# Kernel tuning notes

Measured on AMD Instinct MI355X. Metric: run time of the kernel, lower is better.

## Reference

```python
import jax, jax.numpy as jnp
import numpy as np

BLKQ = 64
BLKK = 64
TOPK_RATIO = 0.125


def setup_inputs() -> dict:
    key = jax.random.key(0)
    ks = jax.random.split(key, 4)
    B, L, H, D = 1, 4096, 16, 64
    q = jax.random.normal(ks[0], (B, L, H, D), jnp.float32)
    k = jax.random.normal(ks[1], (B, L, H, D), jnp.float32)
    v = jax.random.normal(ks[2], (B, L, H, D), jnp.float32)
    w_proj = jax.random.normal(ks[3], (D, D), jnp.float32) * 0.02
    b_proj = jnp.zeros((D,), jnp.float32)
    return {"q": q, "k": k, "v": v, "w_proj": w_proj, "b_proj": b_proj}


def _sparse_linear_attn(q, k, v, w_proj, b_proj):
    # q,k,v: (B, L, H, D) -> (B, H, L, D)
    q = jnp.transpose(q, (0, 2, 1, 3))
    k = jnp.transpose(k, (0, 2, 1, 3))
    v = jnp.transpose(v, (0, 2, 1, 3))
    B, H, L, D = q.shape
    M, N = L // BLKQ, L // BLKK  # L chosen divisible by block sizes (no padding)
    T = max(1, int(TOPK_RATIO * N))  # selected key blocks per query block

    qb = q.reshape(B, H, M, BLKQ, D)
    kb = k.reshape(B, H, N, BLKK, D)
    vb = v.reshape(B, H, N, BLKK, D)

    # --- block map: mean-pooled block descriptors, topk key blocks per query block ---
    qm = qb.mean(axis=3)  # (B,H,M,D)
    km = kb.mean(axis=3)  # (B,H,N,D)
    blk_scores = jnp.einsum('bhmd,bhnd->bhmn', qm, km)
    _, lut = jax.lax.top_k(blk_scores, T)  # (B,H,M,T) int32

    # --- gather selected K/V blocks ---
    b_idx = jnp.arange(B)[:, None, None, None]
    h_idx = jnp.arange(H)[None, :, None, None]
    k_sel = kb[b_idx, h_idx, lut]  # (B,H,M,T,BLKK,D)
    v_sel = vb[b_idx, h_idx, lut]  # (B,H,M,T,BLKK,D)

    # --- block-sparse softmax attention over gathered keys only ---
    scale = D ** (-0.5)
    att = jnp.einsum('bhmqd,bhmtkd->bhmqtk', qb, k_sel) * scale
    att = att.reshape(B, H, M, BLKQ, T * BLKK)
    p = jax.nn.softmax(att, axis=-1)
    o_s = jnp.einsum('bhmqn,bhmnd->bhmqd', p, v_sel.reshape(B, H, M, T * BLKK, D))
    o_s = o_s.reshape(B, H, L, D)

    # --- global linear attention with softmax feature map ---
    q_fm = jax.nn.softmax(q, axis=-1)
    k_fm = jax.nn.softmax(k, axis=-1)
    kvsum = jnp.einsum('bhld,bhle->bhde', k_fm, v)  # (B,H,D,D)
    ksum = k_fm.sum(axis=2)  # (B,H,D)
    num = jnp.einsum('bhld,bhde->bhle', q_fm, kvsum)
    den = jnp.einsum('bhld,bhd->bhl', q_fm, ksum)[..., None] + 1e-6
    o_l = num / den
    o_l = jnp.einsum('bhld,ed->bhle', o_l, w_proj) + b_proj  # nn.Linear: x @ W.T + b

    o = o_s + o_l
    return jnp.transpose(o, (0, 2, 1, 3))  # (B, L, H, D)


def reference(q, k, v, w_proj, b_proj):
    return _sparse_linear_attn(q, k, v, w_proj, b_proj)
```

## Files before the change

kernel.cpp:

```cpp
#include <hip/hip_runtime.h>


#define NH   16
#define DH   64
#define NBLK 64
#define TSEL 8

typedef unsigned short u16;
typedef unsigned int   u32;
typedef __attribute__((ext_vector_type(8))) short short8;
typedef __attribute__((ext_vector_type(4))) float f4;
typedef __attribute__((ext_vector_type(4))) u32 u32x4;

#define MFMA_BF16(a, b, c) __builtin_amdgcn_mfma_f32_16x16x32_bf16(a, b, c, 0, 0, 0)

__device__ __forceinline__ u16 f2bf_rne(float f) {
  u32 u = __float_as_uint(f);
  u += 0x7fffu + ((u >> 16) & 1u);
  return (u16)(u >> 16);
}
__device__ __forceinline__ u32 pk2(float a, float b) {
  return (u32)f2bf_rne(a) | ((u32)f2bf_rne(b) << 16);
}
__device__ __forceinline__ float bf2f(u16 u) { return __uint_as_float(((u32)u) << 16); }

__device__ __forceinline__ short8 frag_row(const u16* t, int row, int jblk) {
  return *(const short8*)((const char*)t + row * 128 + ((jblk ^ (row & 7)) * 16));
}

__global__ __launch_bounds__(256) void prep_kernel(const float* __restrict__ k,
                                                   const float* __restrict__ v,
                                                   u16* __restrict__ kT,
                                                   u16* __restrict__ vT,
                                                   float* __restrict__ kvp,
                                                   float* __restrict__ ksp,
                                                   float* __restrict__ kmv) {
  __shared__ __align__(16) char vsl[8192];
  __shared__ __align__(16) char kfm[8192];
  __shared__ float kcol[64 * 65];
  __shared__ float redmx[256];
  __shared__ float redsm[256];
  __shared__ float kmred[256];
  __shared__ float ksred[256];
  int b = blockIdx.x;
  int n = (b >> 3) & 63;
  int h = 2 * (b & 7) + (b >> 9);
  int tid = threadIdx.x;
  int w = tid >> 6, lane = tid & 63;
  int row = lane, qd = w;
  int lq = lane & 15, quad = lane >> 4;

  float kv[16];
  {
    const float* kr = k + (size_t)(n * 64 + row) * 1024 + h * 64 + qd * 16;
#pragma unroll
    for (int c4 = 0; c4 < 4; c4++) {
      float4 a = *(const float4*)(kr + c4 * 4);
      kv[c4 * 4] = a.x; kv[c4 * 4 + 1] = a.y; kv[c4 * 4 + 2] = a.z; kv[c4 * 4 + 3] = a.w;
    }
  }
  {
    char* ktb = (char*)(kT + ((size_t)(h * 64 + n)) * 4096);
    uint4 w0 = make_uint4(pk2(kv[0], kv[1]), pk2(kv[2], kv[3]),
                          pk2(kv[4], kv[5]), pk2(kv[6], kv[7]));
    uint4 w1 = make_uint4(pk2(kv[8], kv[9]), pk2(kv[10], kv[11]),
                          pk2(kv[12], kv[13]), pk2(kv[14], kv[15]));
    *(uint4*)(ktb + row * 128 + (((2 * qd) ^ (row & 7)) * 16)) = w0;
    *(uint4*)(ktb + row * 128 + (((2 * qd + 1) ^ (row & 7)) * 16)) = w1;
  }
  {
#pragma unroll
    for (int j = 0; j < 16; j++) kcol[(qd * 16 + j) * 65 + row] = kv[j];
  }
  {
    const float* vr = v + (size_t)(n * 64 + row) * 1024 + h * 64 + qd * 16;
    int kb = row >> 3, klo = row & 7;
#pragma unroll
    for (int c4 = 0; c4 < 4; c4++) {
      float4 a = *(const float4*)(vr + c4 * 4);
      float vv[4] = {a.x, a.y, a.z, a.w};
#pragma unroll
      for (int jj = 0; jj < 4; jj++) {
        int e = qd * 16 + c4 * 4 + jj;
        *(u16*)(vsl + e * 128 + ((kb ^ (e & 7)) * 16) + klo * 2) = f2bf_rne(vv[jj]);
      }
    }
  }
  {
    float mx = kv[0];
#pragma unroll
    for (int j = 1; j < 16; j++) mx = fmaxf(mx, kv[j]);
    redmx[qd * 64 + row] = mx;
  }
  __syncthreads();
  {
    int c = tid & 63, g = tid >> 6;
    float pk = 0.f;
#pragma unroll
    for (int i = 0; i < 16; i++) pk += kcol[c * 65 + g * 16 + i];
    kmred[g * 64 + c] = pk;
  }
  {
    float mx = fmaxf(fmaxf(redmx[row], redmx[64 + row]),
                     fmaxf(redmx[128 + row], redmx[192 + row]));
    float sm = 0.f;
#pragma unroll
    for (int j = 0; j < 16; j++) { kv[j] = __expf(kv[j] - mx); sm += kv[j]; }
    redsm[qd * 64 + row] = sm;
  }
  __syncthreads();
  if (tid < 64)
    kmv[h * 4096 + n * 64 + tid] =
        (kmred[tid] + kmred[64 + tid] + kmred[128 + tid] + kmred[192 + tid]) * (1.0f / 64.0f);
  {
    float sm = redsm[row] + redsm[64 + row] + redsm[128 + row] + redsm[192 + row];
    float inv = 1.0f / sm;
    int rb = row >> 3, rlo = row & 7;
#pragma unroll
    for (int j = 0; j < 16; j++) {
      int d = qd * 16 + j;
      *(u16*)(kfm + d * 128 + (((rb) ^ (d & 7)) * 16) + rlo * 2) = f2bf_rne(kv[j] * inv);
    }
  }
  __syncthreads();

  {
    uint4* vt_out = (uint4*)(vT + ((size_t)(h * 64 + n)) * 4096);
    vt_out[tid] = ((const uint4*)vsl)[tid];
    vt_out[256 + tid] = ((const uint4*)vsl)[256 + tid];
  }
  {
    float ks = 0.f;
    short8 x0 = frag_row((const u16*)kfm, lane, 2 * w);
    short8 x1 = frag_row((const u16*)kfm, lane, 2 * w + 1);
#pragma unroll
    for (int e = 0; e < 8; e++) ks += bf2f((u16)x0[e]) + bf2f((u16)x1[e]);
    ksred[tid] = ks;
  }
  {
    f4 acc[4];
    f4 zz = {0.f, 0.f, 0.f, 0.f};
#pragma unroll
    for (int et = 0; et < 4; et++) acc[et] = zz;
#pragma unroll
    for (int ks2 = 0; ks2 < 2; ks2++) {
      short8 a_ = frag_row((const u16*)kfm, w * 16 + lq, 4 * ks2 + quad);
#pragma unroll
      for (int et = 0; et < 4; et++)
        acc[et] = MFMA_BF16(a_, frag_row((const u16*)vsl, et * 16 + lq, 4 * ks2 + quad), acc[et]);
    }
    float* kvb = kvp + ((size_t)(h * 64 + n)) * 4096;
#pragma unroll
    for (int r = 0; r < 4; r++)
#pragma unroll
      for (int et = 0; et < 4; et++)
        kvb[(w * 16 + quad * 4 + r) * 64 + et * 16 + lq] = acc[et][r];
  }
  __syncthreads();
  if (tid < 64)
    ksp[((size_t)(h * 64 + n)) * 64 + tid] = ksred[tid] + ksred[64 + tid] +
                                             ksred[128 + tid] + ksred[192 + tid];
}

__global__ __launch_bounds__(256) void post_kernel(const float* __restrict__ kvp,
                                                   const float* __restrict__ ksp,
                                                   const float* __restrict__ wgt,
                                                   u16* __restrict__ m2t,
                                                   float* __restrict__ ksum) {
  __shared__ float kr[4][64];
  __shared__ float wl[64 * 65];
  int bx = blockIdx.x, tid = threadIdx.x;
  int h = bx >> 4, dq = bx & 15;
  int j = tid & 63, rr = tid >> 6;

  {
    size_t off = (size_t)(dq * 4 + rr) * 64 + j;
    const float* base = kvp + (size_t)h * 64 * 4096 + off;
    float s0 = 0.f, s1 = 0.f, s2 = 0.f, s3 = 0.f;
#pragma unroll
    for (int n4 = 0; n4 < 16; n4++) {
      s0 += base[(size_t)(n4 * 4 + 0) * 4096];
      s1 += base[(size_t)(n4 * 4 + 1) * 4096];
      s2 += base[(size_t)(n4 * 4 + 2) * 4096];
      s3 += base[(size_t)(n4 * 4 + 3) * 4096];
    }
    kr[rr][j] = (s0 + s1) + (s2 + s3);
  }
#pragma unroll
  for (int i = 0; i < 16; i++) {
    int f = i * 256 + tid;
    wl[(f >> 6) * 65 + (f & 63)] = wgt[f];
  }
  __syncthreads();

  {
    int e = tid & 63, rr2 = tid >> 6;
    float acc = 0.f;
#pragma unroll
    for (int jj = 0; jj < 64; jj++) acc = fmaf(kr[rr2][jj], wl[e * 65 + jj], acc);
    int d = dq * 4 + rr2;
    *(u16*)((char*)m2t + (size_t)h * 8192 + e * 128 +
            (((d >> 3) ^ (e & 7)) * 16) + (d & 7) * 2) = f2bf_rne(acc);
  }
  if (dq == 0 && tid < 64) {
    const float* base = ksp + (size_t)h * 64 * 64 + tid;
    float s = 0.f;
#pragma unroll
    for (int n = 0; n < 64; n++) s += base[(size_t)n * 64];
    ksum[h * 64 + tid] = s;
  }
}

__global__ __launch_bounds__(256, 6) void fused_attn_kernel(const float* __restrict__ q,
                                                            const u16* __restrict__ kT,
                                                            const u16* __restrict__ vT,
                                                            const float* __restrict__ kmv,
                                                            const u16* __restrict__ m2t,
                                                            const float* __restrict__ ksum,
                                                            const float* __restrict__ bproj,
                                                            float* __restrict__ out) {
  __shared__ __align__(16) char smem[24576];
  int b = blockIdx.x;
  int m = (b >> 3) & 63;
  int h = 2 * (b & 7) + (b >> 9);
  int tid = threadIdx.x, w = tid >> 6, lane = tid & 63;
  int lq = lane & 15, quad = lane >> 4;
  char* buf = smem;
  char* p_b = smem + 16384 + w * 2048;
  float* km_s = (float*)smem;
  float* qmp = (float*)(smem + 20480);
  float* qmf = (float*)(smem + 21504);

  {
    int c = tid & 63, g = tid >> 6;
    const float* qcol = q + ((size_t)(m * 64 + g * 16)) * 1024 + h * 64 + c;
    float qp = 0.f;
#pragma unroll
    for (int i = 0; i < 16; i++) qp += qcol[(size_t)i * 1024];
    qmp[g * 64 + c] = qp;
#pragma unroll
    for (int i = 0; i < 16; i++) {
      int idx = i * 256 + tid;
      km_s[(idx >> 6) * 65 + (idx & 63)] = kmv[h * 4096 + idx];
    }
  }
  __syncthreads();
  if (tid < 64) qmf[tid] = qmp[tid] + qmp[64 + tid] + qmp[128 + tid] + qmp[192 + tid];
  __syncthreads();
  int blks[8];
  {
    int n = lane;
    float s = 0.f;
#pragma unroll
    for (int d = 0; d < 64; d++) s += qmf[d] * km_s[n * 65 + d];
    float my = s;
#pragma unroll
    for (int t = 0; t < TSEL; t++) {
      float vv = my; int idx = n;
#pragma unroll
      for (int off = 1; off < 64; off <<= 1) {
        float ov = __shfl_xor(vv, off);
        int oi = __shfl_xor(idx, off);
        if (ov > vv || (ov == vv && oi < idx)) { vv = ov; idx = oi; }
      }
      int sel = __builtin_amdgcn_readfirstlane(idx);
      blks[t] = sel;
      if (n == sel) my = -INFINITY;
    }
  }
  __syncthreads();

  const int qrow = w * 16 + lq;
  const float* qr_g = q + ((size_t)(m * 64 + qrow)) * 1024 + h * 64;
  short8 qf[2];
#pragma unroll
  for (int ks = 0; ks < 2; ks++) {
    const float* gp = qr_g + (4 * ks + quad) * 8;
    float4 a = *(const float4*)gp;
    float4 bb = *(const float4*)(gp + 4);
    u32x4 tt = {pk2(a.x, a.y), pk2(a.z, a.w), pk2(bb.x, bb.y), pk2(bb.z, bb.w)};
    qf[ks] = __builtin_bit_cast(short8, tt);
  }

  {
    const uint4* kt0 = (const uint4*)(kT + ((size_t)(h * 64 + blks[0])) * 4096);
    const uint4* vt0 = (const uint4*)(vT + ((size_t)(h * 64 + blks[0])) * 4096);
    ((uint4*)buf)[tid] = kt0[tid];
    ((uint4*)buf)[256 + tid] = kt0[256 + tid];
    ((uint4*)(buf + 8192))[tid] = vt0[tid];
    ((uint4*)(buf + 8192))[256 + tid] = vt0[256 + tid];
  }
  __syncthreads();

  float mrun = -INFINITY, lrun = 0.f;
  f4 o[4];
  f4 zz = {0.f, 0.f, 0.f, 0.f};
#pragma unroll
  for (int et = 0; et < 4; et++) o[et] = zz;

  const u16* kc = (const u16*)buf;
  const u16* vc = (const u16*)(buf + 8192);

  for (int t = 0; t < 8; t++) {
    uint4 pk0, pk1, pv0, pv1;
    if (t < 7) {
      const uint4* ktn = (const uint4*)(kT + ((size_t)(h * 64 + blks[t + 1])) * 4096);
      const uint4* vtn = (const uint4*)(vT + ((size_t)(h * 64 + blks[t + 1])) * 4096);
      pk0 = ktn[tid]; pk1 = ktn[256 + tid];
      pv0 = vtn[tid]; pv1 = vtn[256 + tid];
    }

    f4 s[4];
#pragma unroll
    for (int kt = 0; kt < 4; kt++) s[kt] = zz;
    __builtin_amdgcn_s_setprio(1);
#pragma unroll
    for (int ks = 0; ks < 2; ks++)
#pragma unroll
      for (int kt = 0; kt < 4; kt++)
        s[kt] = MFMA_BF16(frag_row(kc, kt * 16 + lq, 4 * ks + quad), qf[ks], s[kt]);
    __builtin_amdgcn_s_setprio(0);

    float mp = -INFINITY;
#pragma unroll
    for (int kt = 0; kt < 4; kt++)
#pragma unroll
      for (int r = 0; r < 4; r++) mp = fmaxf(mp, s[kt][r]);
    mp = fmaxf(mp, __shfl_xor(mp, 16));
    mp = fmaxf(mp, __shfl_xor(mp, 32));
    mp *= 0.125f;
    if (__any(mp > mrun)) {
      float mn = fmaxf(mrun, mp);
      float al = __expf(mrun - mn);
      mrun = mn;
      lrun *= al;
#pragma unroll
      for (int et = 0; et < 4; et++)
#pragma unroll
        for (int r = 0; r < 4; r++) o[et][r] *= al;
    }
    float rs_ = 0.f;
#pragma unroll
    for (int kt = 0; kt < 4; kt++) {
      float p0 = __expf(fmaf(s[kt][0], 0.125f, -mrun));
      float p1 = __expf(fmaf(s[kt][1], 0.125f, -mrun));
      float p2 = __expf(fmaf(s[kt][2], 0.125f, -mrun));
      float p3 = __expf(fmaf(s[kt][3], 0.125f, -mrun));
      rs_ += p0 + p1 + p2 + p3;
      u32 lo32 = (__float_as_uint(p0) >> 16) | (__float_as_uint(p1) & 0xffff0000u);
      u32 hi32 = (__float_as_uint(p2) >> 16) | (__float_as_uint(p3) & 0xffff0000u);
      int addr = lq * 128 + (((kt * 2 + (quad >> 1)) ^ (lq & 7)) * 16) + (quad & 1) * 8;
      *(uint2*)(p_b + addr) = make_uint2(lo32, hi32);
    }
    rs_ += __shfl_xor(rs_, 16);
    rs_ += __shfl_xor(rs_, 32);
    lrun += rs_;

    __builtin_amdgcn_s_setprio(1);
#pragma unroll
    for (int ks = 0; ks < 2; ks++) {
      short8 pf = frag_row((const u16*)p_b, lq, 4 * ks + quad);
#pragma unroll
      for (int et = 0; et < 4; et++)
        o[et] = MFMA_BF16(frag_row(vc, et * 16 + lq, 4 * ks + quad), pf, o[et]);
    }
    __builtin_amdgcn_s_setprio(0);

    if (t < 7) {
      __syncthreads();
      ((uint4*)buf)[tid] = pk0;
      ((uint4*)buf)[256 + tid] = pk1;
      ((uint4*)(buf + 8192))[tid] = pv0;
      ((uint4*)(buf + 8192))[256 + tid] = pv1;
      __syncthreads();
    }
  }

  __syncthreads();
  {
    const uint4* src = (const uint4*)((const char*)m2t + (size_t)h * 8192);
    ((uint4*)buf)[tid] = src[tid];
    ((uint4*)buf)[256 + tid] = src[256 + tid];
    if (tid < 64) {
      ((float*)(buf + 8192))[tid] = ksum[h * 64 + tid];
      ((float*)(buf + 8448))[tid] = bproj[tid];
    }
  }
  __syncthreads();
  u16* m2_l = (u16*)buf;
  float* ks_s = (float*)(buf + 8192);
  float* b_s = (float*)(buf + 8448);

  float ev[16];
  float mx = -INFINITY;
#pragma unroll
  for (int c4 = 0; c4 < 4; c4++) {
    float4 a = *(const float4*)(qr_g + quad * 16 + c4 * 4);
    ev[c4 * 4] = a.x; ev[c4 * 4 + 1] = a.y; ev[c4 * 4 + 2] = a.z; ev[c4 * 4 + 3] = a.w;
    mx = fmaxf(mx, fmaxf(fmaxf(a.x, a.y), fmaxf(a.z, a.w)));
  }
  mx = fmaxf(mx, __shfl_xor(mx, 16));
  mx = fmaxf(mx, __shfl_xor(mx, 32));
  float sum = 0.f, eks = 0.f;
#pragma unroll
  for (int j = 0; j < 16; j++) {
    float e = __expf(ev[j] - mx);
    ev[j] = e;
    sum += e;
    eks += e * ks_s[quad * 16 + j];
  }
  sum += __shfl_xor(sum, 16); sum += __shfl_xor(sum, 32);
  eks += __shfl_xor(eks, 16); eks += __shfl_xor(eks, 32);
  float invs = 1.0f / sum;
  float den = fmaf(eks, invs, 1e-6f);
  float scale = invs / den;
  uint4 e0v = make_uint4(pk2(ev[0], ev[1]), pk2(ev[2], ev[3]),
                         pk2(ev[4], ev[5]), pk2(ev[6], ev[7]));
  uint4 e1v = make_uint4(pk2(ev[8], ev[9]), pk2(ev[10], ev[11]),
                         pk2(ev[12], ev[13]), pk2(ev[14], ev[15]));
  *(uint4*)(p_b + lq * 128 + (((2 * quad) ^ (lq & 7)) * 16)) = e0v;
  *(uint4*)(p_b + lq * 128 + (((2 * quad + 1) ^ (lq & 7)) * 16)) = e1v;

  f4 oc[4];
  f4 zz2 = {0.f, 0.f, 0.f, 0.f};
#pragma unroll
  for (int et = 0; et < 4; et++) oc[et] = zz2;
  __builtin_amdgcn_s_setprio(1);
#pragma unroll
  for (int ks2 = 0; ks2 < 2; ks2++) {
    short8 ef = frag_row((const u16*)p_b, lq, 4 * ks2 + quad);
#pragma unroll
    for (int et = 0; et < 4; et++)
      oc[et] = MFMA_BF16(frag_row(m2_l, et * 16 + lq, 4 * ks2 + quad), ef, oc[et]);
  }
  __builtin_amdgcn_s_setprio(0);

  float invl = 1.0f / lrun;
  float* gp = out + ((size_t)(m * 64 + qrow)) * 1024 + h * 64 + quad * 4;
#pragma unroll
  for (int et = 0; et < 4; et++) {
    int e0 = et * 16 + quad * 4;
    float4 ov;
    ov.x = o[et][0] * invl + oc[et][0] * scale + b_s[e0 + 0];
    ov.y = o[et][1] * invl + oc[et][1] * scale + b_s[e0 + 1];
    ov.z = o[et][2] * invl + oc[et][2] * scale + b_s[e0 + 2];
    ov.w = o[et][3] * invl + oc[et][3] * scale + b_s[e0 + 3];
    *(float4*)(gp + et * 16) = ov;
  }
}

extern "C" void kernel_launch(void* const* d_in, const int* in_sizes, int n_in,
                              void* d_out, int out_size, void* d_ws, size_t ws_size,
                              hipStream_t stream) {
  const float* q = (const float*)d_in[0];
  const float* k = (const float*)d_in[1];
  const float* v = (const float*)d_in[2];
  const float* w = (const float*)d_in[3];
  const float* b = (const float*)d_in[4];
  float* out = (float*)d_out;

  u16* kT = (u16*)d_ws;
  u16* vT = kT + 4194304;
  float* kvp = (float*)(vT + 4194304);
  float* ksp = kvp + 4194304;
  float* kmv = ksp + 65536;
  float* ksum = kmv + 65536;
  u16* m2t = (u16*)(ksum + 1024);

  prep_kernel<<<1024, 256, 0, stream>>>(k, v, kT, vT, kvp, ksp, kmv);
  post_kernel<<<256, 256, 0, stream>>>(kvp, ksp, w, m2t, ksum);
  fused_attn_kernel<<<1024, 256, 0, stream>>>(q, kT, vT, kmv, m2t, ksum, b, out);
}
```

Before: 137.0 us.

## Fuse post-reduction into attention kernel with magic-flag inter-block sync

Removes the separate post_kernel launch by having the first five m-blocks of each head in the fused attention kernel compute the kv-sum projection and ksum. These blocks publish a magic value to a flag array with release semantics, and all blocks spin on the flags before loading m2t. The change also switches many global loads and stores to nontemporal hints and lowers the occupancy hint from 6 to 4. Flags are never reset, so a later call can read stale magic values from the previous call and skip waiting. The spin is capped, so on timeout results may be silently wrong. The scheme also relies on the producer blocks being scheduled, which is not guaranteed.

```diff
diff --git a/kernel.cpp b/kernel.cpp
--- a/kernel.cpp
+++ b/kernel.cpp
@@ -8,11 +8,14 @@
 
 typedef unsigned short u16;
 typedef unsigned int   u32;
+typedef unsigned long long u64;
 typedef __attribute__((ext_vector_type(8))) short short8;
 typedef __attribute__((ext_vector_type(4))) float f4;
 typedef __attribute__((ext_vector_type(4))) u32 u32x4;
 
 #define MFMA_BF16(a, b, c) __builtin_amdgcn_mfma_f32_16x16x32_bf16(a, b, c, 0, 0, 0)
+#define MAGIC64 0x2468ACE013579BDFull
+#define SPIN_CAP 131072
 
 __device__ __forceinline__ u16 f2bf_rne(float f) {
   u32 u = __float_as_uint(f);
@@ -52,11 +55,11 @@
 
   float kv[16];
   {
-    const float* kr = k + (size_t)(n * 64 + row) * 1024 + h * 64 + qd * 16;
+    const f4* kr = (const f4*)(k + (size_t)(n * 64 + row) * 1024 + h * 64 + qd * 16);
 #pragma unroll
     for (int c4 = 0; c4 < 4; c4++) {
-      float4 a = *(const float4*)(kr + c4 * 4);
-      kv[c4 * 4] = a.x; kv[c4 * 4 + 1] = a.y; kv[c4 * 4 + 2] = a.z; kv[c4 * 4 + 3] = a.w;
+      f4 a = __builtin_nontemporal_load(kr + c4);
+      kv[c4 * 4] = a[0]; kv[c4 * 4 + 1] = a[1]; kv[c4 * 4 + 2] = a[2]; kv[c4 * 4 + 3] = a[3];
     }
   }
   {
@@ -73,12 +76,12 @@
     for (int j = 0; j < 16; j++) kcol[(qd * 16 + j) * 65 + row] = kv[j];
   }
   {
-    const float* vr = v + (size_t)(n * 64 + row) * 1024 + h * 64 + qd * 16;
+    const f4* vr = (const f4*)(v + (size_t)(n * 64 + row) * 1024 + h * 64 + qd * 16);
     int kb = row >> 3, klo = row & 7;
 #pragma unroll
     for (int c4 = 0; c4 < 4; c4++) {
-      float4 a = *(const float4*)(vr + c4 * 4);
-      float vv[4] = {a.x, a.y, a.z, a.w};
+      f4 a = __builtin_nontemporal_load(vr + c4);
+      float vv[4] = {a[0], a[1], a[2], a[3]};
 #pragma unroll
       for (int jj = 0; jj < 4; jj++) {
         int e = qd * 16 + c4 * 4 + jj;
@@ -154,71 +157,28 @@
     for (int r = 0; r < 4; r++)
 #pragma unroll
       for (int et = 0; et < 4; et++)
-        kvb[(w * 16 + quad * 4 + r) * 64 + et * 16 + lq] = acc[et][r];
+        __builtin_nontemporal_store(acc[et][r],
+            kvb + (w * 16 + quad * 4 + r) * 64 + et * 16 + lq);
   }
   __syncthreads();
   if (tid < 64)
-    ksp[((size_t)(h * 64 + n)) * 64 + tid] = ksred[tid] + ksred[64 + tid] +
-                                             ksred[128 + tid] + ksred[192 + tid];
-}
-
-__global__ __launch_bounds__(256) void post_kernel(const float* __restrict__ kvp,
-                                                   const float* __restrict__ ksp,
-                                                   const float* __restrict__ wgt,
-                                                   u16* __restrict__ m2t,
-                                                   float* __restrict__ ksum) {
-  __shared__ float kr[4][64];
-  __shared__ float wl[64 * 65];
-  int bx = blockIdx.x, tid = threadIdx.x;
-  int h = bx >> 4, dq = bx & 15;
-  int j = tid & 63, rr = tid >> 6;
-
-  {
-    size_t off = (size_t)(dq * 4 + rr) * 64 + j;
-    const float* base = kvp + (size_t)h * 64 * 4096 + off;
-    float s0 = 0.f, s1 = 0.f, s2 = 0.f, s3 = 0.f;
-#pragma unroll
-    for (int n4 = 0; n4 < 16; n4++) {
-      s0 += base[(size_t)(n4 * 4 + 0) * 4096];
-      s1 += base[(size_t)(n4 * 4 + 1) * 4096];
-      s2 += base[(size_t)(n4 * 4 + 2) * 4096];
-      s3 += base[(size_t)(n4 * 4 + 3) * 4096];
-    }
-    kr[rr][j] = (s0 + s1) + (s2 + s3);
-  }
-#pragma unroll
-  for (int i = 0; i < 16; i++) {
-    int f = i * 256 + tid;
-    wl[(f >> 6) * 65 + (f & 63)] = wgt[f];
-  }
-  __syncthreads();
-
-  {
-    int e = tid & 63, rr2 = tid >> 6;
-    float acc = 0.f;
-#pragma unroll
-    for (int jj = 0; jj < 64; jj++) acc = fmaf(kr[rr2][jj], wl[e * 65 + jj], acc);
-    int d = dq * 4 + rr2;
-    *(u16*)((char*)m2t + (size_t)h * 8192 + e * 128 +
-            (((d >> 3) ^ (e & 7)) * 16) + (d & 7) * 2) = f2bf_rne(acc);
-  }
-  if (dq == 0 && tid < 64) {
-    const float* base = ksp + (size_t)h * 64 * 64 + tid;
-    float s = 0.f;
-#pragma unroll
-    for (int n = 0; n < 64; n++) s += base[(size_t)n * 64];
-    ksum[h * 64 + tid] = s;
-  }
-}
-
-__global__ __launch_bounds__(256, 6) void fused_attn_kernel(const float* __restrict__ q,
-                                                            const u16* __restrict__ kT,
-                                                            const u16* __restrict__ vT,
-                                                            const float* __restrict__ kmv,
-                                                            const u16* __restrict__ m2t,
-                                                            const float* __restrict__ ksum,
-                                                            const float* __restrict__ bproj,
-                                                            float* __restrict__ out) {
+    __builtin_nontemporal_store(ksred[tid] + ksred[64 + tid] +
+                                ksred[128 + tid] + ksred[192 + tid],
+                                ksp + ((size_t)(h * 64 + n)) * 64 + tid);
+}
+
+__global__ __launch_bounds__(256, 4) void fusedpost_kernel(const float* __restrict__ q,
+                                                           const u16* __restrict__ kT,
+                                                           const u16* __restrict__ vT,
+                                                           const float* __restrict__ kvp,
+                                                           const float* __restrict__ ksp,
+                                                           const float* __restrict__ kmv,
+                                                           const float* __restrict__ wgt,
+                                                           const float* __restrict__ bproj,
+                                                           u16* __restrict__ m2t,
+                                                           float* __restrict__ ksum,
+                                                           u64* __restrict__ mf,
+                                                           float* __restrict__ out) {
   __shared__ __align__(16) char smem[24576];
   int b = blockIdx.x;
   int m = (b >> 3) & 63;
@@ -227,10 +187,64 @@
   int lq = lane & 15, quad = lane >> 4;
   char* buf = smem;
   char* p_b = smem + 16384 + w * 2048;
+
+  if (m < 4) {
+    float* wl = (float*)smem;
+    float* red16 = (float*)(smem + 18048);
+    int j = tid & 63, rr = tid >> 6;
+#pragma unroll
+    for (int i = 0; i < 16; i++) {
+      int f = i * 256 + tid;
+      wl[(f >> 6) * 65 + (f & 63)] = wgt[f];
+    }
+#pragma unroll
+    for (int s = 0; s < 4; s++) {
+      int d = m * 16 + s * 4 + rr;
+      const float* base = kvp + (size_t)h * 64 * 4096 + d * 64 + j;
+      float s0 = 0.f, s1 = 0.f, s2 = 0.f, s3 = 0.f;
+#pragma unroll
+      for (int n4 = 0; n4 < 16; n4++) {
+        s0 += __builtin_nontemporal_load(base + (size_t)(n4 * 4 + 0) * 4096);
+        s1 += __builtin_nontemporal_load(base + (size_t)(n4 * 4 + 1) * 4096);
+        s2 += __builtin_nontemporal_load(base + (size_t)(n4 * 4 + 2) * 4096);
+        s3 += __builtin_nontemporal_load(base + (size_t)(n4 * 4 + 3) * 4096);
+      }
+      red16[(s * 4 + rr) * 64 + j] = (s0 + s1) + (s2 + s3);
+    }
+    __syncthreads();
+    int e = tid & 63, rr2 = tid >> 6;
+#pragma unroll
+    for (int s = 0; s < 4; s++) {
+      int dloc = s * 4 + rr2;
+      float acc = 0.f;
+#pragma unroll
+      for (int jj = 0; jj < 64; jj++)
+        acc = fmaf(red16[dloc * 64 + jj], wl[e * 65 + jj], acc);
+      int d = m * 16 + dloc;
+      *(u16*)((char*)m2t + (size_t)h * 8192 + e * 128 +
+              (((d >> 3) ^ (e & 7)) * 16) + (d & 7) * 2) = f2bf_rne(acc);
+    }
+  } else if (m == 4) {
+    if (tid < 64) {
+      const float* base = ksp + (size_t)h * 64 * 64 + tid;
+      float s = 0.f;
+#pragma unroll
+      for (int n = 0; n < 64; n++) s += __builtin_nontemporal_load(base + (size_t)n * 64);
+      ksum[h * 64 + tid] = s;
+    }
+  }
+  if (m < 5) {
+    __threadfence();
+    __syncthreads();
+    if (tid == 0)
+      __hip_atomic_store(mf + h * 5 + m, MAGIC64, __ATOMIC_RELEASE,
+                         __HIP_MEMORY_SCOPE_AGENT);
+    __syncthreads();
+  }
+
   float* km_s = (float*)smem;
-  float* qmp = (float*)(smem + 20480);
-  float* qmf = (float*)(smem + 21504);
-
+  float* qmp = (float*)(smem + 16640);
+  float* qmf = (float*)(smem + 17664);
   {
     int c = tid & 63, g = tid >> 6;
     const float* qcol = q + ((size_t)(m * 64 + g * 16)) * 1024 + h * 64 + c;
@@ -359,10 +373,10 @@
     __builtin_amdgcn_s_setprio(1);
 #pragma unroll
     for (int ks = 0; ks < 2; ks++) {
-      short8 pf = frag_row((const u16*)p_b, lq, 4 * ks + quad);
+      short8 pfr = frag_row((const u16*)p_b, lq, 4 * ks + quad);
 #pragma unroll
       for (int et = 0; et < 4; et++)
-        o[et] = MFMA_BF16(frag_row(vc, et * 16 + lq, 4 * ks + quad), pf, o[et]);
+        o[et] = MFMA_BF16(frag_row(vc, et * 16 + lq, 4 * ks + quad), pfr, o[et]);
     }
     __builtin_amdgcn_s_setprio(0);
 
@@ -377,6 +391,16 @@
   }
 
   __syncthreads();
+  if (tid < 5) {
+    const u64* fp1 = mf + h * 5 + tid;
+    int c = 0;
+    while (__hip_atomic_load(fp1, __ATOMIC_RELAXED, __HIP_MEMORY_SCOPE_AGENT) != MAGIC64) {
+      if (++c > SPIN_CAP) break;
+      __builtin_amdgcn_s_sleep(8);
+    }
+  }
+  __syncthreads();
+  __builtin_amdgcn_fence(__ATOMIC_ACQUIRE, "agent");
   {
     const uint4* src = (const uint4*)((const char*)m2t + (size_t)h * 8192);
     ((uint4*)buf)[tid] = src[tid];
@@ -440,12 +464,12 @@
 #pragma unroll
   for (int et = 0; et < 4; et++) {
     int e0 = et * 16 + quad * 4;
-    float4 ov;
-    ov.x = o[et][0] * invl + oc[et][0] * scale + b_s[e0 + 0];
-    ov.y = o[et][1] * invl + oc[et][1] * scale + b_s[e0 + 1];
-    ov.z = o[et][2] * invl + oc[et][2] * scale + b_s[e0 + 2];
-    ov.w = o[et][3] * invl + oc[et][3] * scale + b_s[e0 + 3];
-    *(float4*)(gp + et * 16) = ov;
+    f4 ov;
+    ov[0] = o[et][0] * invl + oc[et][0] * scale + b_s[e0 + 0];
+    ov[1] = o[et][1] * invl + oc[et][1] * scale + b_s[e0 + 1];
+    ov[2] = o[et][2] * invl + oc[et][2] * scale + b_s[e0 + 2];
+    ov[3] = o[et][3] * invl + oc[et][3] * scale + b_s[e0 + 3];
+    __builtin_nontemporal_store(ov, (f4*)(gp + et * 16));
   }
 }
 
@@ -466,8 +490,9 @@
   float* kmv = ksp + 65536;
   float* ksum = kmv + 65536;
   u16* m2t = (u16*)(ksum + 1024);
+  u64* mf = (u64*)(m2t + 65536);
 
   prep_kernel<<<1024, 256, 0, stream>>>(k, v, kT, vT, kvp, ksp, kmv);
-  post_kernel<<<256, 256, 0, stream>>>(kvp, ksp, w, m2t, ksum);
-  fused_attn_kernel<<<1024, 256, 0, stream>>>(q, kT, vT, kmv, m2t, ksum, b, out);
-}
+  fusedpost_kernel<<<1024, 256, 0, stream>>>(q, kT, vT, kvp, ksp, kmv, w, b,
+                                             m2t, ksum, mf, out);
+}
```

Result: slower. 246.5 us (+80.0%).
